# Kernel optimization log

Measured on AMD Instinct MI355X. Metric: run time of the kernel, lower is better.

The kernel has to match this reference:

```python
import jax, jax.numpy as jnp
from jax import lax
import numpy as np

S, B, XD = 2048, 64, 64   # seq_len, batch, x_dim
DX = 128                   # dense_x[-1]
H = 256                    # dim_RNN
DH = 128                   # dense_h_x[-1]
ALPHAS = np.array([0.9, 0.5, 0.1, 0.01], dtype=np.float32)


def setup_inputs() -> dict:
    key = jax.random.key(0)
    ks = jax.random.split(key, 12)
    def lin(k, fan_in, shape):
        return jax.random.normal(k, shape, jnp.float32) / np.sqrt(fan_in)
    sigmas = jnp.asarray(-np.log(1.0 / ALPHAS - 1.0), jnp.float32)  # inverse sigmoid
    return {
        "x": jax.random.normal(ks[0], (S, B, XD), jnp.float32),
        "Wx": lin(ks[1], XD, (XD, DX)),   # feature_extractor_x linear
        "bx": jnp.zeros((DX,), jnp.float32),
        "Wih": lin(ks[2], DX, (H, DX)),   # RNN input-hidden
        "bih": jnp.zeros((H,), jnp.float32),
        "Whh": lin(ks[3], H, (H, H)),     # RNN hidden-hidden
        "bhh": jnp.zeros((H,), jnp.float32),
        "Whx": lin(ks[4], H, (H, DH)),    # mlp_h_x linear
        "bhx": jnp.zeros((DH,), jnp.float32),
        "Wout": lin(ks[5], DH, (DH, XD)), # gen_out
        "bout": jnp.zeros((XD,), jnp.float32),
        "sigmas": sigmas,
    }


def reference(x, Wx, bx, Wih, bih, Whh, bhh, Whx, bhx, Wout, bout, sigmas):
    # alphas_per_unit: sigmoid(sigmas) tiled to dim_RNN
    alphas = jnp.tile(jax.nn.sigmoid(sigmas), H // sigmas.shape[0])  # [H]
    # feature extractor over all timesteps (teacher forcing, mix_ratio=0)
    feat = jnp.tanh(x @ Wx + bx)  # [S, B, DX]
    h0 = jnp.zeros((x.shape[1], H), x.dtype)

    def step(h, f_t):
        # emit y_t from previous hidden state: gen_out(tanh(mlp_h_x(h)))
        y_t = jnp.tanh(h @ Whx + bhx) @ Wout + bout        # [B, XD]
        # single-step Elman RNN cell
        h_new = jnp.tanh(f_t @ Wih.T + bih + h @ Whh.T + bhh)
        # leaky integration blend per unit
        h_next = (1.0 - alphas) * h + alphas * h_new
        return h_next, y_t

    _, y = lax.scan(step, h0, feat)  # y: [S, B, XD]
    return y
```

## Files before the change

kernel.cpp:

```cpp
#include <hip/hip_runtime.h>
#include <math.h>

#define SS 2048
#define BB 64
#define XDIM 64
#define DXF 128
#define HH 256
#define DHH 128

typedef float v2f __attribute__((ext_vector_type(2)));

__device__ __forceinline__ float ftanh(float x) {
    float e = __expf(2.0f * x);
    return 1.0f - 2.0f / (e + 1.0f);
}

template <int CTRL>
__device__ __forceinline__ float dpp_mov_f(float x) {
    return __int_as_float(__builtin_amdgcn_update_dpp(
        0, __float_as_int(x), CTRL, 0xF, 0xF, true));
}
#define RED8_SHR(s) { s += dpp_mov_f<0x111>(s); s += dpp_mov_f<0x112>(s); \
                      s += dpp_mov_f<0x114>(s); }
#define RED8_SHL(s) { s += dpp_mov_f<0x101>(s); s += dpp_mov_f<0x102>(s); \
                      s += dpp_mov_f<0x104>(s); }

__global__ __launch_bounds__(256) void k1_featu(
    const float* __restrict__ x, const float* __restrict__ Wx,
    const float* __restrict__ bx, const float* __restrict__ Wih,
    const float* __restrict__ bih, const float* __restrict__ bhh,
    float* __restrict__ u)
{
    __shared__ float xs[64][XDIM];
    __shared__ float fs[64][DXF];
    const int tid = threadIdx.x;
    const size_t row0 = (size_t)blockIdx.x * 64;

    for (int v = tid; v < 64 * XDIM; v += 256) {
        int r = v >> 6, m = v & 63;
        xs[r][m] = x[(row0 + r) * XDIM + m];
    }
    __syncthreads();

    {
        const int cq = tid & 31;
        const int ru = tid >> 5;
        v2f aA[2][4], aB[2][4];
        #pragma unroll
        for (int g = 0; g < 2; ++g)
            #pragma unroll
            for (int i = 0; i < 4; ++i) { aA[g][i] = (v2f)0.f; aB[g][i] = (v2f)0.f; }

        #pragma unroll
        for (int kc = 0; kc < 4; ++kc) {
            v2f wA[16], wB[16];
            #pragma unroll
            for (int k = 0; k < 16; ++k) {
                const float* wp = Wx + (kc * 16 + k) * DXF + cq;
                wA[k] = (v2f){wp[0],  wp[32]};
                wB[k] = (v2f){wp[64], wp[96]};
            }
            #pragma unroll
            for (int g = 0; g < 2; ++g) {
                const int rb = 8 * ru + 4 * g;
                #pragma unroll
                for (int k4 = 0; k4 < 4; ++k4) {
                    float4 xv[4];
                    #pragma unroll
                    for (int i = 0; i < 4; ++i)
                        xv[i] = *(const float4*)&xs[rb + i][kc * 16 + 4 * k4];
                    #pragma unroll
                    for (int i = 0; i < 4; ++i) {
                        #pragma unroll
                        for (int e = 0; e < 4; ++e) {
                            const float xe = (e == 0) ? xv[i].x : (e == 1) ? xv[i].y
                                           : (e == 2) ? xv[i].z : xv[i].w;
                            const v2f xb = (v2f){xe, xe};
                            aA[g][i] += wA[4 * k4 + e] * xb;
                            aB[g][i] += wB[4 * k4 + e] * xb;
                        }
                    }
                }
            }
        }
        const float b0 = bx[cq], b1 = bx[cq + 32], b2 = bx[cq + 64], b3 = bx[cq + 96];
        #pragma unroll
        for (int g = 0; g < 2; ++g)
            #pragma unroll
            for (int i = 0; i < 4; ++i) {
                const int r = 8 * ru + 4 * g + i;
                fs[r][cq]      = ftanh(aA[g][i].x + b0);
                fs[r][cq + 32] = ftanh(aA[g][i].y + b1);
                fs[r][cq + 64] = ftanh(aB[g][i].x + b2);
                fs[r][cq + 96] = ftanh(aB[g][i].y + b3);
            }
    }
    __syncthreads();

    {
        const int q4 = tid & 63;
        const int rq = tid >> 6;
        v2f aA[4][4], aB[4][4];
        #pragma unroll
        for (int g = 0; g < 4; ++g)
            #pragma unroll
            for (int i = 0; i < 4; ++i) { aA[g][i] = (v2f)0.f; aB[g][i] = (v2f)0.f; }

        #pragma unroll
        for (int kc = 0; kc < 8; ++kc) {
            v2f wA[16], wB[16];
            #pragma unroll
            for (int k4 = 0; k4 < 4; ++k4) {
                const float4 w0 = *(const float4*)(Wih + (size_t)(q4      ) * DXF + kc * 16 + 4 * k4);
                const float4 w1 = *(const float4*)(Wih + (size_t)(q4 +  64) * DXF + kc * 16 + 4 * k4);
                const float4 w2 = *(const float4*)(Wih + (size_t)(q4 + 128) * DXF + kc * 16 + 4 * k4);
                const float4 w3 = *(const float4*)(Wih + (size_t)(q4 + 192) * DXF + kc * 16 + 4 * k4);
                wA[4 * k4 + 0] = (v2f){w0.x, w1.x}; wA[4 * k4 + 1] = (v2f){w0.y, w1.y};
                wA[4 * k4 + 2] = (v2f){w0.z, w1.z}; wA[4 * k4 + 3] = (v2f){w0.w, w1.w};
                wB[4 * k4 + 0] = (v2f){w2.x, w3.x}; wB[4 * k4 + 1] = (v2f){w2.y, w3.y};
                wB[4 * k4 + 2] = (v2f){w2.z, w3.z}; wB[4 * k4 + 3] = (v2f){w2.w, w3.w};
            }
            #pragma unroll
            for (int g = 0; g < 4; ++g) {
                const int rb = 16 * rq + 4 * g;
                #pragma unroll
                for (int k4 = 0; k4 < 4; ++k4) {
                    float4 fv[4];
                    #pragma unroll
                    for (int i = 0; i < 4; ++i)
                        fv[i] = *(const float4*)&fs[rb + i][kc * 16 + 4 * k4];
                    #pragma unroll
                    for (int i = 0; i < 4; ++i) {
                        #pragma unroll
                        for (int e = 0; e < 4; ++e) {
                            const float fe = (e == 0) ? fv[i].x : (e == 1) ? fv[i].y
                                           : (e == 2) ? fv[i].z : fv[i].w;
                            const v2f fb = (v2f){fe, fe};
                            aA[g][i] += wA[4 * k4 + e] * fb;
                            aB[g][i] += wB[4 * k4 + e] * fb;
                        }
                    }
                }
            }
        }
        const float b0 = bih[q4]       + bhh[q4];
        const float b1 = bih[q4 + 64]  + bhh[q4 + 64];
        const float b2 = bih[q4 + 128] + bhh[q4 + 128];
        const float b3 = bih[q4 + 192] + bhh[q4 + 192];
        #pragma unroll
        for (int g = 0; g < 4; ++g)
            #pragma unroll
            for (int i = 0; i < 4; ++i) {
                const size_t row = row0 + 16 * rq + 4 * g + i;
                u[row * HH + q4]       = aA[g][i].x + b0;
                u[row * HH + q4 + 64]  = aA[g][i].y + b1;
                u[row * HH + q4 + 128] = aB[g][i].x + b2;
                u[row * HH + q4 + 192] = aB[g][i].y + b3;
            }
    }
}

__global__ __launch_bounds__(1024, 4) void k2_rnn(
    const float* __restrict__ u, const float* __restrict__ Whh,
    const float* __restrict__ sigmas, float* __restrict__ hist)
{
    __shared__ float hbuf[2][HH];
    const int tid = threadIdx.x;
    const int b = blockIdx.x;
    const int c = tid & 7;
    const int rg = tid >> 3;

    v2f w2[2][16];
    #pragma unroll
    for (int r = 0; r < 2; ++r) {
        const float* wrow = Whh + (size_t)(2 * rg + r) * HH + 32 * c;
        #pragma unroll
        for (int j = 0; j < 8; ++j) {
            const int kk = 4 * ((j + c) & 7);
            const float4 wv = *(const float4*)(wrow + kk);
            w2[r][2 * j]     = (v2f){wv.x, wv.y};
            w2[r][2 * j + 1] = (v2f){wv.z, wv.w};
        }
    }

    const bool updHi = (c == 7);
    const bool updLo = (c == 0);
    const bool upd = updHi || updLo;
    const int myrow = 2 * rg + (updHi ? 0 : 1);

    const float alpha = 1.f / (1.f + __expf(-sigmas[myrow & 3]));

    if (tid < HH) hbuf[0][tid] = 0.0f;

    float ucur = 0.f;
    if (upd) ucur = u[(size_t)b * HH + myrow];
    __syncthreads();

    for (int t = 0; t < SS; ++t) {
        const int cur = t & 1;
        const int nxt = cur ^ 1;
        const size_t base = ((size_t)t * BB + b) * HH;

        float unext = ucur;
        if (upd) {
            const int tn = (t + 1 < SS) ? (t + 1) : t;
            unext = u[((size_t)tn * BB + b) * HH + myrow];
        }

        v2f a0 = (v2f)0.f, a1 = (v2f)0.f;
        const float4* h4p = (const float4*)&hbuf[cur][32 * c];
        #pragma unroll
        for (int j = 0; j < 8; ++j) {
            const float4 h4 = h4p[(j + c) & 7];
            const v2f hA = (v2f){h4.x, h4.y};
            const v2f hB = (v2f){h4.z, h4.w};
            a0 += w2[0][2 * j] * hA; a0 += w2[0][2 * j + 1] * hB;
            a1 += w2[1][2 * j] * hA; a1 += w2[1][2 * j + 1] * hB;
        }
        float s0 = a0.x + a0.y;
        float s1 = a1.x + a1.y;
        RED8_SHR(s0)
        RED8_SHL(s1)

        if (upd) {
            const float s = (updHi ? s0 : s1) + ucur;
            const float hold = hbuf[cur][myrow];
            hist[base + myrow] = hold;
            hbuf[nxt][myrow] = hold + alpha * (ftanh(s) - hold);
            ucur = unext;
        }
        __syncthreads();
    }
}

__global__ __launch_bounds__(256) void k3_y(
    const float* __restrict__ hist, const float* __restrict__ Whx,
    const float* __restrict__ bhx, const float* __restrict__ Wout,
    const float* __restrict__ bout, float* __restrict__ y)
{
    __shared__ float hs[32][HH];
    __shared__ float gs[32][DHH];
    const int tid = threadIdx.x;
    const size_t row0 = (size_t)blockIdx.x * 32;

    for (int v = tid; v < 32 * HH; v += 256) {
        int r = v >> 8, i = v & 255;
        hs[r][i] = hist[(row0 + r) * HH + i];
    }
    __syncthreads();

    {
        const int aq = tid & 31;
        const int ru = tid >> 5;
        v2f aA[4], aB[4];
        #pragma unroll
        for (int i = 0; i < 4; ++i) { aA[i] = (v2f)0.f; aB[i] = (v2f)0.f; }

        #pragma unroll
        for (int kc = 0; kc < 16; ++kc) {
            v2f wA[16], wB[16];
            #pragma unroll
            for (int k = 0; k < 16; ++k) {
                const float* wp = Whx + (size_t)(kc * 16 + k) * DHH + aq;
                wA[k] = (v2f){wp[0],  wp[32]};
                wB[k] = (v2f){wp[64], wp[96]};
            }
            #pragma unroll
            for (int k4 = 0; k4 < 4; ++k4) {
                float4 hv[4];
                #pragma unroll
                for (int i = 0; i < 4; ++i)
                    hv[i] = *(const float4*)&hs[4 * ru + i][kc * 16 + 4 * k4];
                #pragma unroll
                for (int i = 0; i < 4; ++i) {
                    #pragma unroll
                    for (int e = 0; e < 4; ++e) {
                        const float he = (e == 0) ? hv[i].x : (e == 1) ? hv[i].y
                                       : (e == 2) ? hv[i].z : hv[i].w;
                        const v2f hb = (v2f){he, he};
                        aA[i] += wA[4 * k4 + e] * hb;
                        aB[i] += wB[4 * k4 + e] * hb;
                    }
                }
            }
        }
        const float b0 = bhx[aq], b1 = bhx[aq + 32], b2 = bhx[aq + 64], b3 = bhx[aq + 96];
        #pragma unroll
        for (int i = 0; i < 4; ++i) {
            const int r = 4 * ru + i;
            gs[r][aq]      = ftanh(aA[i].x + b0);
            gs[r][aq + 32] = ftanh(aA[i].y + b1);
            gs[r][aq + 64] = ftanh(aB[i].x + b2);
            gs[r][aq + 96] = ftanh(aB[i].y + b3);
        }
    }
    __syncthreads();

    {
        const int o2 = tid & 31;
        const int ru = tid >> 5;
        v2f acc[4];
        #pragma unroll
        for (int i = 0; i < 4; ++i) acc[i] = (v2f)0.f;

        #pragma unroll
        for (int kc = 0; kc < 2; ++kc) {
            v2f w[64];
            #pragma unroll
            for (int k = 0; k < 64; ++k) {
                const float* wp = Wout + (size_t)(kc * 64 + k) * XDIM + o2;
                w[k] = (v2f){wp[0], wp[32]};
            }
            #pragma unroll
            for (int k4 = 0; k4 < 16; ++k4) {
                float4 gv[4];
                #pragma unroll
                for (int i = 0; i < 4; ++i)
                    gv[i] = *(const float4*)&gs[4 * ru + i][kc * 64 + 4 * k4];
                #pragma unroll
                for (int i = 0; i < 4; ++i) {
                    #pragma unroll
                    for (int e = 0; e < 4; ++e) {
                        const float ge = (e == 0) ? gv[i].x : (e == 1) ? gv[i].y
                                       : (e == 2) ? gv[i].z : gv[i].w;
                        acc[i] += w[4 * k4 + e] * (v2f){ge, ge};
                    }
                }
            }
        }
        const float b0 = bout[o2], b1 = bout[o2 + 32];
        #pragma unroll
        for (int i = 0; i < 4; ++i) {
            const size_t row = row0 + 4 * ru + i;
            y[row * XDIM + o2]      = acc[i].x + b0;
            y[row * XDIM + o2 + 32] = acc[i].y + b1;
        }
    }
}

extern "C" void kernel_launch(void* const* d_in, const int* in_sizes, int n_in,
                              void* d_out, int out_size, void* d_ws, size_t ws_size,
                              hipStream_t stream) {
    const float* x      = (const float*)d_in[0];
    const float* Wx     = (const float*)d_in[1];
    const float* bx     = (const float*)d_in[2];
    const float* Wih    = (const float*)d_in[3];
    const float* bih    = (const float*)d_in[4];
    const float* Whh    = (const float*)d_in[5];
    const float* bhh    = (const float*)d_in[6];
    const float* Whx    = (const float*)d_in[7];
    const float* bhx    = (const float*)d_in[8];
    const float* Wout   = (const float*)d_in[9];
    const float* bout   = (const float*)d_in[10];
    const float* sigmas = (const float*)d_in[11];
    float* y = (float*)d_out;

    float* u    = (float*)d_ws;
    float* hist = u + (size_t)SS * BB * HH;

    k1_featu<<<(SS * BB) / 64, 256, 0, stream>>>(x, Wx, bx, Wih, bih, bhh, u);
    k2_rnn<<<BB, 1024, 0, stream>>>(u, Whh, sigmas, hist);
    k3_y<<<(SS * BB) / 32, 256, 0, stream>>>(hist, Whx, bhx, Wout, bout, y);
}
```

Before: 2.088 ms.

## Repartition RNN recurrence: 16 lanes per 4 rows with 16-lane DPP reduction

Changes the k2_rnn work split so each group of 16 lanes computes 4 hidden rows over 16-column chunks, instead of 8 lanes computing 2 rows over 32-column chunks. Each thread now holds 4x16 weights, the same register count as before, but every LDS read of h is reused across 4 rows. The DPP reduction gains a fourth stage. The edge lanes update two adjacent rows with vectorised u loads and hist/hbuf stores. The goal is fewer LDS reads per FMA and fewer updating threads, at the cost of a longer reduction chain and more reduction instructions per step.

```diff
diff --git a/kernel.cpp b/kernel.cpp
--- a/kernel.cpp
+++ b/kernel.cpp
@@ -20,10 +20,10 @@
     return __int_as_float(__builtin_amdgcn_update_dpp(
         0, __float_as_int(x), CTRL, 0xF, 0xF, true));
 }
-#define RED8_SHR(s) { s += dpp_mov_f<0x111>(s); s += dpp_mov_f<0x112>(s); \
-                      s += dpp_mov_f<0x114>(s); }
-#define RED8_SHL(s) { s += dpp_mov_f<0x101>(s); s += dpp_mov_f<0x102>(s); \
-                      s += dpp_mov_f<0x104>(s); }
+#define RED_SHR(s) { s += dpp_mov_f<0x111>(s); s += dpp_mov_f<0x112>(s); \
+                     s += dpp_mov_f<0x114>(s); s += dpp_mov_f<0x118>(s); }
+#define RED_SHL(s) { s += dpp_mov_f<0x101>(s); s += dpp_mov_f<0x102>(s); \
+                     s += dpp_mov_f<0x104>(s); s += dpp_mov_f<0x108>(s); }
 
 __global__ __launch_bounds__(256) void k1_featu(
     const float* __restrict__ x, const float* __restrict__ Wx,
@@ -167,33 +167,41 @@
     __shared__ float hbuf[2][HH];
     const int tid = threadIdx.x;
     const int b = blockIdx.x;
-    const int c = tid & 7;
-    const int rg = tid >> 3;
-
-    v2f w2[2][16];
+    const int c = tid & 15;
+    const int rg = tid >> 4;
+    const int sw = c >> 1;
+
+    v2f w2[4][8];
     #pragma unroll
-    for (int r = 0; r < 2; ++r) {
-        const float* wrow = Whh + (size_t)(2 * rg + r) * HH + 32 * c;
-        #pragma unroll
-        for (int j = 0; j < 8; ++j) {
-            const int kk = 4 * ((j + c) & 7);
-            const float4 wv = *(const float4*)(wrow + kk);
+    for (int r = 0; r < 4; ++r) {
+        const float* wrow = Whh + (size_t)(4 * rg + r) * HH + 16 * c;
+        #pragma unroll
+        for (int j = 0; j < 4; ++j) {
+            const int m = (j + sw) & 3;
+            const float4 wv = *(const float4*)(wrow + 4 * m);
             w2[r][2 * j]     = (v2f){wv.x, wv.y};
             w2[r][2 * j + 1] = (v2f){wv.z, wv.w};
         }
     }
-
-    const bool updHi = (c == 7);
+    #pragma unroll
+    for (int r = 0; r < 4; ++r)
+        asm volatile("" : "+v"(w2[r][0]), "+v"(w2[r][1]), "+v"(w2[r][2]),
+                          "+v"(w2[r][3]), "+v"(w2[r][4]), "+v"(w2[r][5]),
+                          "+v"(w2[r][6]), "+v"(w2[r][7]));
+
+    const bool updHi = (c == 15);
     const bool updLo = (c == 0);
     const bool upd = updHi || updLo;
-    const int myrow = 2 * rg + (updHi ? 0 : 1);
-
-    const float alpha = 1.f / (1.f + __expf(-sigmas[myrow & 3]));
+    const int r0 = 4 * rg + (updHi ? 0 : 2);
+
+    v2f alpha2;
+    alpha2.x = 1.f / (1.f + __expf(-sigmas[updHi ? 0 : 2]));
+    alpha2.y = 1.f / (1.f + __expf(-sigmas[updHi ? 1 : 3]));
 
     if (tid < HH) hbuf[0][tid] = 0.0f;
 
-    float ucur = 0.f;
-    if (upd) ucur = u[(size_t)b * HH + myrow];
+    v2f ucur = (v2f)0.f;
+    if (upd) ucur = *(const v2f*)&u[(size_t)b * HH + r0];
     __syncthreads();
 
     for (int t = 0; t < SS; ++t) {
@@ -201,32 +209,38 @@
         const int nxt = cur ^ 1;
         const size_t base = ((size_t)t * BB + b) * HH;
 
-        float unext = ucur;
+        v2f unext = ucur;
         if (upd) {
             const int tn = (t + 1 < SS) ? (t + 1) : t;
-            unext = u[((size_t)tn * BB + b) * HH + myrow];
-        }
-
-        v2f a0 = (v2f)0.f, a1 = (v2f)0.f;
-        const float4* h4p = (const float4*)&hbuf[cur][32 * c];
-        #pragma unroll
-        for (int j = 0; j < 8; ++j) {
-            const float4 h4 = h4p[(j + c) & 7];
+            unext = *(const v2f*)&u[((size_t)tn * BB + b) * HH + r0];
+        }
+
+        v2f a0 = (v2f)0.f, a1 = (v2f)0.f, a2 = (v2f)0.f, a3 = (v2f)0.f;
+        const float4* hp = (const float4*)&hbuf[cur][16 * c];
+        #pragma unroll
+        for (int j = 0; j < 4; ++j) {
+            const float4 h4 = hp[(j + sw) & 3];
             const v2f hA = (v2f){h4.x, h4.y};
             const v2f hB = (v2f){h4.z, h4.w};
             a0 += w2[0][2 * j] * hA; a0 += w2[0][2 * j + 1] * hB;
             a1 += w2[1][2 * j] * hA; a1 += w2[1][2 * j + 1] * hB;
-        }
-        float s0 = a0.x + a0.y;
-        float s1 = a1.x + a1.y;
-        RED8_SHR(s0)
-        RED8_SHL(s1)
+            a2 += w2[2][2 * j] * hA; a2 += w2[2][2 * j + 1] * hB;
+            a3 += w2[3][2 * j] * hA; a3 += w2[3][2 * j + 1] * hB;
+        }
+        float s0 = a0.x + a0.y, s1 = a1.x + a1.y;
+        float s2 = a2.x + a2.y, s3 = a3.x + a3.y;
+        RED_SHR(s0) RED_SHR(s1)
+        RED_SHL(s2) RED_SHL(s3)
 
         if (upd) {
-            const float s = (updHi ? s0 : s1) + ucur;
-            const float hold = hbuf[cur][myrow];
-            hist[base + myrow] = hold;
-            hbuf[nxt][myrow] = hold + alpha * (ftanh(s) - hold);
+            v2f sv = updHi ? (v2f){s0, s1} : (v2f){s2, s3};
+            sv += ucur;
+            const v2f hold = *(const v2f*)&hbuf[cur][r0];
+            *(v2f*)&hist[base + r0] = hold;
+            v2f hnew;
+            hnew.x = hold.x + alpha2.x * (ftanh(sv.x) - hold.x);
+            hnew.y = hold.y + alpha2.y * (ftanh(sv.y) - hold.y);
+            *(v2f*)&hbuf[nxt][r0] = hnew;
             ucur = unext;
         }
         __syncthreads();
```

Measured after the change: 2.515 ms. 1.2x slower.

## Rewrite RNN recurrence kernel in inline assembly with 16-lane row split

Applied to the files above, without the earlier changes.

Replaces the k2_rnn recurrence loop with hand-written GCN inline assembly. Each 16-lane group now computes four output rows over 16-float column chunks. Lane 15 writes two rows and lane 0 writes the other two, using paired dword loads and stores. Partial sums are reduced with DPP row shifts, and LDS pointers are double-buffered by XOR so the per-step barrier path stays short. The aim is to shorten the serial per-timestep critical path. In exchange the code is hard to maintain, clobbers about 120 VGPRs, bakes in fixed layout assumptions, and a pointer or exec-mask mistake would produce wrong results.

```diff
diff --git a/kernel.cpp b/kernel.cpp
--- a/kernel.cpp
+++ b/kernel.cpp
@@ -14,16 +14,6 @@
     float e = __expf(2.0f * x);
     return 1.0f - 2.0f / (e + 1.0f);
 }
-
-template <int CTRL>
-__device__ __forceinline__ float dpp_mov_f(float x) {
-    return __int_as_float(__builtin_amdgcn_update_dpp(
-        0, __float_as_int(x), CTRL, 0xF, 0xF, true));
-}
-#define RED8_SHR(s) { s += dpp_mov_f<0x111>(s); s += dpp_mov_f<0x112>(s); \
-                      s += dpp_mov_f<0x114>(s); }
-#define RED8_SHL(s) { s += dpp_mov_f<0x101>(s); s += dpp_mov_f<0x102>(s); \
-                      s += dpp_mov_f<0x104>(s); }
 
 __global__ __launch_bounds__(256) void k1_featu(
     const float* __restrict__ x, const float* __restrict__ Wx,
@@ -160,77 +150,234 @@
     }
 }
 
-__global__ __launch_bounds__(1024, 4) void k2_rnn(
+__global__ __launch_bounds__(1024) void k2_rnn(
     const float* __restrict__ u, const float* __restrict__ Whh,
     const float* __restrict__ sigmas, float* __restrict__ hist)
 {
     __shared__ float hbuf[2][HH];
     const int tid = threadIdx.x;
     const int b = blockIdx.x;
-    const int c = tid & 7;
-    const int rg = tid >> 3;
-
-    v2f w2[2][16];
-    #pragma unroll
-    for (int r = 0; r < 2; ++r) {
-        const float* wrow = Whh + (size_t)(2 * rg + r) * HH + 32 * c;
-        #pragma unroll
-        for (int j = 0; j < 8; ++j) {
-            const int kk = 4 * ((j + c) & 7);
-            const float4 wv = *(const float4*)(wrow + kk);
-            w2[r][2 * j]     = (v2f){wv.x, wv.y};
-            w2[r][2 * j + 1] = (v2f){wv.z, wv.w};
-        }
-    }
-
-    const bool updHi = (c == 7);
-    const bool updLo = (c == 0);
-    const bool upd = updHi || updLo;
-    const int myrow = 2 * rg + (updHi ? 0 : 1);
-
-    const float alpha = 1.f / (1.f + __expf(-sigmas[myrow & 3]));
-
-    if (tid < HH) hbuf[0][tid] = 0.0f;
-
-    float ucur = 0.f;
-    if (upd) ucur = u[(size_t)b * HH + myrow];
-    __syncthreads();
-
-    for (int t = 0; t < SS; ++t) {
-        const int cur = t & 1;
-        const int nxt = cur ^ 1;
-        const size_t base = ((size_t)t * BB + b) * HH;
-
-        float unext = ucur;
-        if (upd) {
-            const int tn = (t + 1 < SS) ? (t + 1) : t;
-            unext = u[((size_t)tn * BB + b) * HH + myrow];
-        }
-
-        v2f a0 = (v2f)0.f, a1 = (v2f)0.f;
-        const float4* h4p = (const float4*)&hbuf[cur][32 * c];
-        #pragma unroll
-        for (int j = 0; j < 8; ++j) {
-            const float4 h4 = h4p[(j + c) & 7];
-            const v2f hA = (v2f){h4.x, h4.y};
-            const v2f hB = (v2f){h4.z, h4.w};
-            a0 += w2[0][2 * j] * hA; a0 += w2[0][2 * j + 1] * hB;
-            a1 += w2[1][2 * j] * hA; a1 += w2[1][2 * j + 1] * hB;
-        }
-        float s0 = a0.x + a0.y;
-        float s1 = a1.x + a1.y;
-        RED8_SHR(s0)
-        RED8_SHL(s1)
-
-        if (upd) {
-            const float s = (updHi ? s0 : s1) + ucur;
-            const float hold = hbuf[cur][myrow];
-            hist[base + myrow] = hold;
-            hbuf[nxt][myrow] = hold + alpha * (ftanh(s) - hold);
-            ucur = unext;
-        }
-        __syncthreads();
-    }
+
+    const bool hi = ((tid & 15) == 15);
+    const float ax = 1.f / (1.f + __expf(-sigmas[hi ? 0 : 2]));
+    const float ay = 1.f / (1.f + __expf(-sigmas[hi ? 1 : 3]));
+
+    const float* ub = u + (size_t)b * HH;
+    float* hb = hist + (size_t)b * HH;
+    const unsigned ulo = (unsigned)(uintptr_t)ub;
+    const unsigned uhi = (unsigned)((uintptr_t)ub >> 32);
+    const unsigned hlo = (unsigned)(uintptr_t)hb;
+    const unsigned hhi = (unsigned)((uintptr_t)hb >> 32);
+    const unsigned wlo = (unsigned)(uintptr_t)Whh;
+    const unsigned whi = (unsigned)((uintptr_t)Whh >> 32);
+    const unsigned lb  = (unsigned)(uintptr_t)(void*)&hbuf[0][0];
+
+    asm volatile(
+        "v_and_b32 v106, 15, %[tid]\n\t"
+        "v_lshrrev_b32 v107, 4, %[tid]\n\t"
+        "v_lshrrev_b32 v108, 1, v106\n\t"
+        "v_and_b32 v108, 3, v108\n\t"
+        "v_lshlrev_b32 v109, 6, v106\n\t"
+        "v_lshlrev_b32 v110, 4, v108\n\t"
+        "v_add_u32 v90, v109, v110\n\t"
+        "v_add_u32 v110, 1, v108\n\t"
+        "v_and_b32 v110, 3, v110\n\t"
+        "v_lshlrev_b32 v110, 4, v110\n\t"
+        "v_add_u32 v91, v109, v110\n\t"
+        "v_add_u32 v110, 2, v108\n\t"
+        "v_and_b32 v110, 3, v110\n\t"
+        "v_lshlrev_b32 v110, 4, v110\n\t"
+        "v_add_u32 v92, v109, v110\n\t"
+        "v_add_u32 v110, 3, v108\n\t"
+        "v_and_b32 v110, 3, v110\n\t"
+        "v_lshlrev_b32 v110, 4, v110\n\t"
+        "v_add_u32 v93, v109, v110\n\t"
+        "v_lshlrev_b32 v114, 12, v107\n\t"
+        "v_add_u32 v115, v114, v90\n\t"
+        "v_mov_b32 v113, %[whi]\n\t"
+        "v_add_co_u32 v112, vcc, %[wlo], v115\n\t"
+        "v_addc_co_u32 v113, vcc, 0, v113, vcc\n\t"
+        "global_load_dwordx4 v[0:3], v[112:113], off\n\t"
+        "global_load_dwordx4 v[16:19], v[112:113], off offset:1024\n\t"
+        "global_load_dwordx4 v[32:35], v[112:113], off offset:2048\n\t"
+        "global_load_dwordx4 v[48:51], v[112:113], off offset:3072\n\t"
+        "v_add_u32 v115, v114, v91\n\t"
+        "v_mov_b32 v113, %[whi]\n\t"
+        "v_add_co_u32 v112, vcc, %[wlo], v115\n\t"
+        "v_addc_co_u32 v113, vcc, 0, v113, vcc\n\t"
+        "global_load_dwordx4 v[4:7], v[112:113], off\n\t"
+        "global_load_dwordx4 v[20:23], v[112:113], off offset:1024\n\t"
+        "global_load_dwordx4 v[36:39], v[112:113], off offset:2048\n\t"
+        "global_load_dwordx4 v[52:55], v[112:113], off offset:3072\n\t"
+        "v_add_u32 v115, v114, v92\n\t"
+        "v_mov_b32 v113, %[whi]\n\t"
+        "v_add_co_u32 v112, vcc, %[wlo], v115\n\t"
+        "v_addc_co_u32 v113, vcc, 0, v113, vcc\n\t"
+        "global_load_dwordx4 v[8:11], v[112:113], off\n\t"
+        "global_load_dwordx4 v[24:27], v[112:113], off offset:1024\n\t"
+        "global_load_dwordx4 v[40:43], v[112:113], off offset:2048\n\t"
+        "global_load_dwordx4 v[56:59], v[112:113], off offset:3072\n\t"
+        "v_add_u32 v115, v114, v93\n\t"
+        "v_mov_b32 v113, %[whi]\n\t"
+        "v_add_co_u32 v112, vcc, %[wlo], v115\n\t"
+        "v_addc_co_u32 v113, vcc, 0, v113, vcc\n\t"
+        "global_load_dwordx4 v[12:15], v[112:113], off\n\t"
+        "global_load_dwordx4 v[28:31], v[112:113], off offset:1024\n\t"
+        "global_load_dwordx4 v[44:47], v[112:113], off offset:2048\n\t"
+        "global_load_dwordx4 v[60:63], v[112:113], off offset:3072\n\t"
+        "v_add_u32 v90, %[lb], v90\n\t"
+        "v_add_u32 v91, %[lb], v91\n\t"
+        "v_add_u32 v92, %[lb], v92\n\t"
+        "v_add_u32 v93, %[lb], v93\n\t"
+        "v_add_u32 v110, 1, v106\n\t"
+        "v_lshrrev_b32 v110, 3, v110\n\t"
+        "v_and_b32 v110, 2, v110\n\t"
+        "v_sub_u32 v110, 2, v110\n\t"
+        "v_lshlrev_b32 v111, 2, v107\n\t"
+        "v_add_u32 v111, v111, v110\n\t"
+        "v_lshlrev_b32 v115, 2, v111\n\t"
+        "v_add_u32 v94, 0x400, v115\n\t"
+        "v_add_u32 v94, %[lb], v94\n\t"
+        "v_mov_b32 v99, %[uhi]\n\t"
+        "v_add_co_u32 v98, vcc, %[ulo], v115\n\t"
+        "v_addc_co_u32 v99, vcc, 0, v99, vcc\n\t"
+        "v_mov_b32 v97, %[hhi]\n\t"
+        "v_add_co_u32 v96, vcc, %[hlo], v115\n\t"
+        "v_addc_co_u32 v97, vcc, 0, v97, vcc\n\t"
+        "global_load_dwordx2 v[104:105], v[98:99], off\n\t"
+        "v_lshlrev_b32 v116, 4, v107\n\t"
+        "v_add_u32 v116, %[lb], v116\n\t"
+        "v_mov_b32 v118, 0\n\t"
+        "v_mov_b32 v119, 0\n\t"
+        "ds_write_b64 v116, v[118:119]\n\t"
+        "ds_write_b64 v116, v[118:119] offset:8\n\t"
+        "v_mov_b32 v100, 0\n\t"
+        "v_mov_b32 v101, 0\n\t"
+        "v_mov_b32 v102, %[ax]\n\t"
+        "v_mov_b32 v103, %[ay]\n\t"
+        "s_mov_b32 s20, 0x80018001\n\t"
+        "s_mov_b32 s21, 0x80018001\n\t"
+        "s_mov_b32 s24, 0x4038aa3b\n\t"
+        "s_mov_b32 s25, 0x800\n\t"
+        "s_waitcnt vmcnt(0) lgkmcnt(0)\n\t"
+        "s_barrier\n\t"
+        "Lk2loop_%=:\n\t"
+        "ds_read_b128 v[64:67], v90\n\t"
+        "ds_read_b128 v[68:71], v91\n\t"
+        "ds_read_b128 v[72:75], v92\n\t"
+        "ds_read_b128 v[76:79], v93\n\t"
+        "s_waitcnt lgkmcnt(0)\n\t"
+        "v_pk_mul_f32 v[80:81], v[0:1], v[64:65]\n\t"
+        "v_pk_mul_f32 v[82:83], v[16:17], v[64:65]\n\t"
+        "v_pk_mul_f32 v[84:85], v[32:33], v[64:65]\n\t"
+        "v_pk_mul_f32 v[86:87], v[48:49], v[64:65]\n\t"
+        "v_pk_fma_f32 v[80:81], v[2:3], v[66:67], v[80:81]\n\t"
+        "v_pk_fma_f32 v[82:83], v[18:19], v[66:67], v[82:83]\n\t"
+        "v_pk_fma_f32 v[84:85], v[34:35], v[66:67], v[84:85]\n\t"
+        "v_pk_fma_f32 v[86:87], v[50:51], v[66:67], v[86:87]\n\t"
+        "v_pk_fma_f32 v[80:81], v[4:5], v[68:69], v[80:81]\n\t"
+        "v_pk_fma_f32 v[82:83], v[20:21], v[68:69], v[82:83]\n\t"
+        "v_pk_fma_f32 v[84:85], v[36:37], v[68:69], v[84:85]\n\t"
+        "v_pk_fma_f32 v[86:87], v[52:53], v[68:69], v[86:87]\n\t"
+        "v_pk_fma_f32 v[80:81], v[6:7], v[70:71], v[80:81]\n\t"
+        "v_pk_fma_f32 v[82:83], v[22:23], v[70:71], v[82:83]\n\t"
+        "v_pk_fma_f32 v[84:85], v[38:39], v[70:71], v[84:85]\n\t"
+        "v_pk_fma_f32 v[86:87], v[54:55], v[70:71], v[86:87]\n\t"
+        "v_pk_fma_f32 v[80:81], v[8:9], v[72:73], v[80:81]\n\t"
+        "v_pk_fma_f32 v[82:83], v[24:25], v[72:73], v[82:83]\n\t"
+        "v_pk_fma_f32 v[84:85], v[40:41], v[72:73], v[84:85]\n\t"
+        "v_pk_fma_f32 v[86:87], v[56:57], v[72:73], v[86:87]\n\t"
+        "v_pk_fma_f32 v[80:81], v[10:11], v[74:75], v[80:81]\n\t"
+        "v_pk_fma_f32 v[82:83], v[26:27], v[74:75], v[82:83]\n\t"
+        "v_pk_fma_f32 v[84:85], v[42:43], v[74:75], v[84:85]\n\t"
+        "v_pk_fma_f32 v[86:87], v[58:59], v[74:75], v[86:87]\n\t"
+        "v_pk_fma_f32 v[80:81], v[12:13], v[76:77], v[80:81]\n\t"
+        "v_pk_fma_f32 v[82:83], v[28:29], v[76:77], v[82:83]\n\t"
+        "v_pk_fma_f32 v[84:85], v[44:45], v[76:77], v[84:85]\n\t"
+        "v_pk_fma_f32 v[86:87], v[60:61], v[76:77], v[86:87]\n\t"
+        "v_pk_fma_f32 v[80:81], v[14:15], v[78:79], v[80:81]\n\t"
+        "v_pk_fma_f32 v[82:83], v[30:31], v[78:79], v[82:83]\n\t"
+        "v_pk_fma_f32 v[84:85], v[46:47], v[78:79], v[84:85]\n\t"
+        "v_pk_fma_f32 v[86:87], v[62:63], v[78:79], v[86:87]\n\t"
+        "v_add_f32 v108, v80, v81\n\t"
+        "v_add_f32 v109, v82, v83\n\t"
+        "v_add_f32 v110, v84, v85\n\t"
+        "v_add_f32 v111, v86, v87\n\t"
+        "v_add_f32 v108, v108, v108 row_shr:1 bound_ctrl:0\n\t"
+        "v_add_f32 v109, v109, v109 row_shr:1 bound_ctrl:0\n\t"
+        "v_add_f32 v110, v110, v110 row_shl:1 bound_ctrl:0\n\t"
+        "v_add_f32 v111, v111, v111 row_shl:1 bound_ctrl:0\n\t"
+        "v_add_f32 v108, v108, v108 row_shr:2 bound_ctrl:0\n\t"
+        "v_add_f32 v109, v109, v109 row_shr:2 bound_ctrl:0\n\t"
+        "v_add_f32 v110, v110, v110 row_shl:2 bound_ctrl:0\n\t"
+        "v_add_f32 v111, v111, v111 row_shl:2 bound_ctrl:0\n\t"
+        "v_add_f32 v108, v108, v108 row_shr:4 bound_ctrl:0\n\t"
+        "v_add_f32 v109, v109, v109 row_shr:4 bound_ctrl:0\n\t"
+        "v_add_f32 v110, v110, v110 row_shl:4 bound_ctrl:0\n\t"
+        "v_add_f32 v111, v111, v111 row_shl:4 bound_ctrl:0\n\t"
+        "v_add_f32 v108, v108, v108 row_shr:8 bound_ctrl:0\n\t"
+        "v_add_f32 v109, v109, v109 row_shr:8 bound_ctrl:0\n\t"
+        "v_add_f32 v110, v110, v110 row_shl:8 bound_ctrl:0\n\t"
+        "v_add_f32 v111, v111, v111 row_shl:8 bound_ctrl:0\n\t"
+        "v_cmp_eq_u32 vcc, 15, v106\n\t"
+        "v_cndmask_b32 v112, v110, v108, vcc\n\t"
+        "v_cndmask_b32 v113, v111, v109, vcc\n\t"
+        "s_and_saveexec_b64 s[22:23], s[20:21]\n\t"
+        "s_waitcnt vmcnt(0)\n\t"
+        "v_add_f32 v112, v112, v104\n\t"
+        "v_add_f32 v113, v113, v105\n\t"
+        "v_mul_f32 v114, s24, v112\n\t"
+        "v_mul_f32 v115, s24, v113\n\t"
+        "v_exp_f32 v114, v114\n\t"
+        "v_exp_f32 v115, v115\n\t"
+        "v_add_f32 v114, 1.0, v114\n\t"
+        "v_add_f32 v115, 1.0, v115\n\t"
+        "v_rcp_f32 v114, v114\n\t"
+        "v_rcp_f32 v115, v115\n\t"
+        "v_fma_f32 v114, -2.0, v114, 1.0\n\t"
+        "v_fma_f32 v115, -2.0, v115, 1.0\n\t"
+        "v_mov_b32 v116, v100\n\t"
+        "v_mov_b32 v117, v101\n\t"
+        "global_store_dwordx2 v[96:97], v[116:117], off\n\t"
+        "v_sub_f32 v114, v114, v100\n\t"
+        "v_sub_f32 v115, v115, v101\n\t"
+        "v_fmac_f32 v100, v102, v114\n\t"
+        "v_fmac_f32 v101, v103, v115\n\t"
+        "ds_write_b64 v94, v[100:101]\n\t"
+        "v_add_co_u32 v98, vcc, 0x10000, v98\n\t"
+        "v_addc_co_u32 v99, vcc, 0, v99, vcc\n\t"
+        "global_load_dwordx2 v[104:105], v[98:99], off\n\t"
+        "v_add_co_u32 v96, vcc, 0x10000, v96\n\t"
+        "v_addc_co_u32 v97, vcc, 0, v97, vcc\n\t"
+        "s_mov_b64 exec, s[22:23]\n\t"
+        "v_xor_b32 v90, 0x400, v90\n\t"
+        "v_xor_b32 v91, 0x400, v91\n\t"
+        "v_xor_b32 v92, 0x400, v92\n\t"
+        "v_xor_b32 v93, 0x400, v93\n\t"
+        "v_xor_b32 v94, 0x400, v94\n\t"
+        "s_waitcnt lgkmcnt(0)\n\t"
+        "s_barrier\n\t"
+        "s_sub_u32 s25, s25, 1\n\t"
+        "s_cmp_lg_u32 s25, 0\n\t"
+        "s_cbranch_scc1 Lk2loop_%=\n\t"
+        :
+        : [tid]"v"(tid), [ax]"v"(ax), [ay]"v"(ay), [lb]"v"(lb),
+          [ulo]"s"(ulo), [uhi]"s"(uhi), [hlo]"s"(hlo), [hhi]"s"(hhi),
+          [wlo]"s"(wlo), [whi]"s"(whi)
+        : "memory", "vcc", "scc", "s20", "s21", "s22", "s23", "s24", "s25",
+          "v0","v1","v2","v3","v4","v5","v6","v7","v8","v9",
+          "v10","v11","v12","v13","v14","v15","v16","v17","v18","v19",
+          "v20","v21","v22","v23","v24","v25","v26","v27","v28","v29",
+          "v30","v31","v32","v33","v34","v35","v36","v37","v38","v39",
+          "v40","v41","v42","v43","v44","v45","v46","v47","v48","v49",
+          "v50","v51","v52","v53","v54","v55","v56","v57","v58","v59",
+          "v60","v61","v62","v63","v64","v65","v66","v67","v68","v69",
+          "v70","v71","v72","v73","v74","v75","v76","v77","v78","v79",
+          "v80","v81","v82","v83","v84","v85","v86","v87","v88","v89",
+          "v90","v91","v92","v93","v94","v95","v96","v97","v98","v99",
+          "v100","v101","v102","v103","v104","v105","v106","v107","v108","v109",
+          "v110","v111","v112","v113","v114","v115","v116","v117","v118","v119"
+    );
 }
 
 __global__ __launch_bounds__(256) void k3_y(
```

Measured after the change: 2.139 ms. 1.02x slower.
